# Optimization experiments

Hardware: AMD Instinct MI355X
Metric: run time of the kernel (lower is better)

The kernel has to match this reference:

```python
import jax, jax.numpy as jnp
import numpy as np

IM = 256          # image size (square)
GRID = 512        # oversampled NUFFT grid
J = 6             # Kaiser-Bessel kernel width (torchkbnufft default numpoints)
ALPHA = GRID / IM
BETA = float(np.pi * np.sqrt((J / ALPHA) ** 2 * (ALPHA - 0.5) ** 2 - 0.8))  # Fessler 'best' beta
SC0 = float(np.sinh(BETA) / BETA)
B, C = 1, 8
N_SPOKES, N_SAMPLES = 256, 512
K = N_SPOKES * N_SAMPLES


def _scale_2d():
    # deapodization (inverse FT of KB kernel), separable, normalized to 1 at center
    n = (jnp.arange(IM) - IM / 2) / GRID
    t = BETA ** 2 - (np.pi * J * n) ** 2
    sp = jnp.sqrt(jnp.maximum(t, 1e-12))
    sn = jnp.sqrt(jnp.maximum(-t, 1e-12))
    ft = jnp.where(t > 0, jnp.sinh(sp) / sp, jnp.sinc(sn / np.pi))
    sc = (SC0 / ft).astype(jnp.float32)
    return sc[:, None] * sc[None, :]  # (IM, IM)


def _interp_coords(ktraj):
    # ktraj (2, K) in [-pi, pi] -> J neighbor grid indices + KB weights per dim
    tm = ktraj * (GRID / (2.0 * np.pi))
    base = jnp.floor(tm - J / 2.0)
    j = jnp.arange(1, J + 1, dtype=tm.dtype)
    idx = base[:, :, None] + j                     # (2, K, J)
    u = tm[:, :, None] - idx                       # kernel-centered distance
    q = jnp.maximum(1.0 - (2.0 * u / J) ** 2, 0.0)
    w = jnp.i0(BETA * jnp.sqrt(q)) / J             # (2, K, J) KB weights
    gi = jnp.mod(idx, GRID).astype(jnp.int32)
    return gi[0], gi[1], w[0], w[1]                # iy, ix, wy, wx


def _nufft_fwd(img, coords, sc2):
    # img (B, C, IM, IM) complex -> (B, C, K) non-uniform k-space, 'ortho' norm
    iy, ix, wy, wx = coords
    pad = jnp.zeros(img.shape[:2] + (GRID, GRID), img.dtype)
    pad = pad.at[..., :IM, :IM].set(img * sc2)
    kg = jnp.fft.fft2(pad) / GRID                  # /sqrt(GRID*GRID)
    vals = kg[..., iy[:, :, None], ix[:, None, :]]           # (B,C,K,J,J)
    w2 = (wy[:, :, None] * wx[:, None, :]).astype(kg.dtype)  # (K,J,J)
    return jnp.sum(vals * w2, axis=(-2, -1))


def _nufft_adj(kdata, coords, sc2, smaps):
    # kdata (B, C, K) -> coil-combined image (B, 1, IM, IM), 'ortho' norm
    iy, ix, wy, wx = coords
    w2 = (wy[:, :, None] * wx[:, None, :]).astype(kdata.dtype)
    vals = (kdata[..., None, None] * w2).reshape(kdata.shape[:2] + (-1,))
    flat = (iy[:, :, None] * GRID + ix[:, None, :]).reshape(-1)
    grid = jnp.zeros(kdata.shape[:2] + (GRID * GRID,), kdata.dtype)
    grid = grid.at[:, :, flat].add(vals).reshape(kdata.shape[:2] + (GRID, GRID))
    img = jnp.fft.ifft2(grid) * GRID               # adjoint of fft2/GRID
    img = img[..., :IM, :IM] * sc2
    return jnp.sum(jnp.conj(smaps) * img, axis=1, keepdims=True)


def setup_inputs() -> dict:
    key = jax.random.key(0)
    ks = jax.random.split(key, 6)
    # golden-angle radial trajectory (2, K) in [-pi, pi]
    ga = np.pi * (3.0 - np.sqrt(5.0))
    ang = np.arange(N_SPOKES) * ga
    r = np.linspace(-np.pi, np.pi, N_SAMPLES, endpoint=False)
    ky = np.outer(np.sin(ang), r).reshape(-1)
    kx = np.outer(np.cos(ang), r).reshape(-1)
    ktraj = jnp.asarray(np.stack([ky, kx]), dtype=jnp.float32)
    return {
        "x": jax.random.normal(ks[0], (B, 1, IM, IM), jnp.float32),
        "y_real": jax.random.normal(ks[1], (B, C, K), jnp.float32),
        "y_imag": jax.random.normal(ks[2], (B, C, K), jnp.float32),
        "smaps_real": jax.random.normal(ks[3], (B, C, IM, IM), jnp.float32),
        "smaps_imag": jax.random.normal(ks[4], (B, C, IM, IM), jnp.float32),
        "ktraj": ktraj,
        "lambda_raw": jnp.full((1,), float(np.log(np.exp(1.0) - 1.0)), jnp.float32),
    }


def reference(x, y_real, y_imag, smaps_real, smaps_imag, ktraj, lambda_raw):
    sc2 = _scale_2d()
    coords = _interp_coords(ktraj)
    smaps = (smaps_real + 1j * smaps_imag).astype(jnp.complex64)
    y = (y_real + 1j * y_imag).astype(jnp.complex64)
    x_c = x.astype(jnp.complex64)
    coil_images = x_c * smaps                      # (B, C, IM, IM)
    A_x = _nufft_fwd(coil_images, coords, sc2)     # (B, C, K)
    lam = jax.nn.sigmoid(lambda_raw)[0].astype(jnp.complex64)
    k_dc = lam * A_x + (1.0 - lam) * y             # data consistency mix
    return _nufft_adj(k_dc, coords, sc2, smaps)    # (B, 1, IM, IM) complex64
```

## Files before the change

### kernel.cpp

```cpp
#include <hip/hip_runtime.h>
#include <math.h>

#define GRID_N 512
#define IM_N   256
#define NCOIL  8
#define NK     131072
#define PLANE  (GRID_N*GRID_N)
#define JW     6
#define NBIN   (GRID_N*GRID_N/512*512)
#define WSZ    11
#define NWIN   47
#define ACCROWS 528
#define BETA_F 13.8551003f
#define KSCALE 81.48733086305042f

struct cplx { float x, y; };

__device__ __forceinline__ float bessel_i0f(float x){
  if (x < 3.75f){
    float t = x*(1.0f/3.75f); t = t*t;
    return 1.0f + t*(3.5156229f + t*(3.0899424f + t*(1.2067492f
           + t*(0.2659732f + t*(0.0360768f + t*0.0045813f)))));
  } else {
    float t = 3.75f/x;
    float p = 0.39894228f + t*(0.01328592f + t*(0.00225319f + t*(-0.00157565f
            + t*(0.00916281f + t*(-0.02057706f + t*(0.02635537f
            + t*(-0.01647633f + t*0.00392377f)))))));
    return p * __expf(x) * rsqrtf(x);
  }
}

__device__ __forceinline__ float kb_w(float u){
  float uu = u*(1.0f/3.0f);
  float q = fmaxf(1.0f - uu*uu, 0.0f);
  return bessel_i0f(BETA_F*sqrtf(q)) * (1.0f/6.0f);
}

__device__ __forceinline__ unsigned bf16_of(float f){
  unsigned u = __float_as_uint(f);
  return (u + 0x8000u) >> 16;
}
__device__ __forceinline__ float bf_lo(unsigned w){ return __uint_as_float(w << 16); }
__device__ __forceinline__ float bf_hi(unsigned w){ return __uint_as_float(w & 0xFFFF0000u); }

__global__ void k_sc_table(float* sc){
  int i = threadIdx.x;
  if (i >= IM_N) return;
  float n  = (i - IM_N*0.5f) * (1.0f/GRID_N);
  float pj = 3.14159265358979f * (float)JW * n;
  float t  = BETA_F*BETA_F - pj*pj;
  float sp = sqrtf(fmaxf(t, 1e-12f));
  float sn = sqrtf(fmaxf(-t, 1e-12f));
  float ft = (t > 0.0f) ? (sinhf(sp)/sp) : (sinf(sn)/sn);
  float sc0 = sinhf(BETA_F)/BETA_F;
  sc[i] = sc0/ft;
}

__global__ void k_zero1(float* p, int n){
  int i = blockIdx.x*blockDim.x + threadIdx.x;
  if (i < n) p[i] = 0.f;
}

__global__ void k_fft_fill(const float* __restrict__ ximg, const float* __restrict__ sr,
                           const float* __restrict__ si, const float* __restrict__ sc,
                           cplx* __restrict__ buf){
  __shared__ cplx lds[GRID_N];
  int blk = blockIdx.x;
  int c = blk >> 9, y = blk & (GRID_N-1);
  cplx* p = buf + (size_t)blk * GRID_N;
  int tid = threadIdx.x;
  if (y >= IM_N){
    cplx z; z.x = 0.f; z.y = 0.f;
    for (int i = tid; i < GRID_N; i += 256) p[i] = z;
    return;
  }
  float scy = sc[y];
  for (int i = tid; i < GRID_N; i += 256){
    int r = __brev((unsigned)i) >> 23;
    cplx v; v.x = 0.f; v.y = 0.f;
    if (i < IM_N){
      float vv = ximg[(y<<8)|i] * scy * sc[i];
      int gi = (c << 16) | (y << 8) | i;
      v.x = vv * sr[gi]; v.y = vv * si[gi];
    }
    lds[r] = v;
  }
  __syncthreads();
  for (int half = 1; half < GRID_N; half <<= 1){
    int j = tid & (half-1);
    int k = ((tid & ~(half-1)) << 1) | j;
    float ang = -3.14159265358979f * (float)j / (float)half;
    float sw, cw; __sincosf(ang, &sw, &cw);
    cplx u = lds[k];
    cplx v = lds[k+half];
    cplx t; t.x = v.x*cw - v.y*sw; t.y = v.x*sw + v.y*cw;
    lds[k].x      = u.x + t.x; lds[k].y      = u.y + t.y;
    lds[k+half].x = u.x - t.x; lds[k+half].y = u.y - t.y;
    __syncthreads();
  }
  for (int i = tid; i < GRID_N; i += 256) p[i] = lds[i];
}

template<int DIR>
__global__ void k_fft_rows(cplx* __restrict__ buf, float scale){
  __shared__ cplx lds[GRID_N];
  cplx* p = buf + (size_t)blockIdx.x * GRID_N;
  int tid = threadIdx.x;
  for (int i = tid; i < GRID_N; i += 256){
    int r = __brev((unsigned)i) >> 23;
    lds[r] = p[i];
  }
  __syncthreads();
  for (int half = 1; half < GRID_N; half <<= 1){
    int j = tid & (half-1);
    int k = ((tid & ~(half-1)) << 1) | j;
    float ang = (float)DIR * 3.14159265358979f * (float)j / (float)half;
    float sw, cw; __sincosf(ang, &sw, &cw);
    cplx u = lds[k];
    cplx v = lds[k+half];
    cplx t; t.x = v.x*cw - v.y*sw; t.y = v.x*sw + v.y*cw;
    lds[k].x      = u.x + t.x; lds[k].y      = u.y + t.y;
    lds[k+half].x = u.x - t.x; lds[k+half].y = u.y - t.y;
    __syncthreads();
  }
  for (int i = tid; i < GRID_N; i += 256){
    cplx v = lds[i]; v.x *= scale; v.y *= scale; p[i] = v;
  }
}

__global__ void k_fft_rows_c(cplx* __restrict__ buf, float scale){
  __shared__ cplx lds[GRID_N];
  int b = blockIdx.x;
  int c = b >> 8, y = b & (IM_N-1);
  cplx* p = buf + (size_t)c*PLANE + (size_t)y*GRID_N;
  int tid = threadIdx.x;
  for (int i = tid; i < GRID_N; i += 256){
    int r = __brev((unsigned)i) >> 23;
    lds[r] = p[i];
  }
  __syncthreads();
  for (int half = 1; half < GRID_N; half <<= 1){
    int j = tid & (half-1);
    int k = ((tid & ~(half-1)) << 1) | j;
    float ang = 3.14159265358979f * (float)j / (float)half;
    float sw, cw; __sincosf(ang, &sw, &cw);
    cplx u = lds[k];
    cplx v = lds[k+half];
    cplx t; t.x = v.x*cw - v.y*sw; t.y = v.x*sw + v.y*cw;
    lds[k].x      = u.x + t.x; lds[k].y      = u.y + t.y;
    lds[k+half].x = u.x - t.x; lds[k+half].y = u.y - t.y;
    __syncthreads();
  }
  for (int i = tid; i < IM_N; i += 256){
    cplx v = lds[i]; v.x *= scale; v.y *= scale; p[i] = v;
  }
}

__global__ void k_transpose(const cplx* __restrict__ in, cplx* __restrict__ out){
  __shared__ cplx tile[32][33];
  int c  = blockIdx.z;
  int x0 = blockIdx.x*32, y0 = blockIdx.y*32;
  const cplx* ip = in  + (size_t)c*PLANE;
  cplx*       op = out + (size_t)c*PLANE;
  int tx = threadIdx.x, ty = threadIdx.y;
  for (int dy = 0; dy < 32; dy += 8)
    tile[ty+dy][tx] = ip[(size_t)(y0+ty+dy)*GRID_N + (x0+tx)];
  __syncthreads();
  for (int dy = 0; dy < 32; dy += 8)
    op[(size_t)(x0+ty+dy)*GRID_N + (y0+tx)] = tile[tx][ty+dy];
}

__global__ void k_c2i(const float2* __restrict__ plan, float2* __restrict__ inter){
  int t = blockIdx.x*blockDim.x + threadIdx.x;
  if (t >= PLANE*NCOIL) return;
  int c = t & 7; int cell = t >> 3;
  inter[(size_t)cell*8 + c] = plan[(size_t)c*PLANE + cell];
}

__global__ __launch_bounds__(256) void k_fwd(
    const float* __restrict__ ktraj, const float* __restrict__ yre,
    const float* __restrict__ yim, const float* __restrict__ lraw,
    const float4* __restrict__ KTi4, float4* __restrict__ kdc4){
  int t = blockIdx.x*blockDim.x + threadIdx.x;
  if (t >= NK*4) return;
  int k = t >> 2, p = t & 3;

  int iy[JW], ix[JW]; float wy[JW], wx[JW];
  {
    float tm = ktraj[k] * KSCALE;
    int base = (int)floorf(tm - 3.0f);
    #pragma unroll
    for (int j = 1; j <= JW; ++j){
      int fidx = base + j;
      wy[j-1] = kb_w(tm - (float)fidx);
      iy[j-1] = fidx & (GRID_N-1);
    }
  }
  {
    float tm = ktraj[NK + k] * KSCALE;
    int base = (int)floorf(tm - 3.0f);
    #pragma unroll
    for (int j = 1; j <= JW; ++j){
      int fidx = base + j;
      wx[j-1] = kb_w(tm - (float)fidx);
      ix[j-1] = fidx & (GRID_N-1);
    }
  }

  float ax=0.f, ay=0.f, az=0.f, aw=0.f;
  #pragma unroll
  for (int jx = 0; jx < JW; ++jx){
    int ox = ix[jx]*GRID_N;
    #pragma unroll
    for (int jy = 0; jy < JW; ++jy){
      float w2 = wx[jx]*wy[jy];
      float4 v = KTi4[(size_t)(ox + iy[jy])*4 + p];
      ax += w2*v.x; ay += w2*v.y; az += w2*v.z; aw += w2*v.w;
    }
  }
  float lam = 1.0f/(1.0f + __expf(-lraw[0]));
  float oml = 1.0f - lam;
  int c0 = 2*p;
  float4 o;
  o.x = lam*ax + oml*yre[(size_t)c0*NK + k];
  o.y = lam*ay + oml*yim[(size_t)c0*NK + k];
  o.z = lam*az + oml*yre[(size_t)(c0+1)*NK + k];
  o.w = lam*aw + oml*yim[(size_t)(c0+1)*NK + k];
  kdc4[(size_t)k*4 + p] = o;
}

__global__ void k_hist2(const float* __restrict__ ktraj, unsigned* __restrict__ hist2){
  int k = blockIdx.x*blockDim.x + threadIdx.x;
  if (k >= NK) return;
  float tmy = ktraj[k] * KSCALE;
  int by = ((int)floorf(tmy - 3.0f)) & (GRID_N-1);
  float tmx = ktraj[NK + k] * KSCALE;
  int bx = (int)floorf(tmx - 3.0f);
  #pragma unroll
  for (int j = 1; j <= JW; ++j){
    int cj = (bx + j) & (GRID_N-1);
    atomicAdd(&hist2[cj*GRID_N + by], 1u);
  }
}

__global__ void k_colscan(const unsigned* __restrict__ hist2,
                          unsigned* __restrict__ binOff,
                          unsigned* __restrict__ colTotal){
  __shared__ unsigned s[GRID_N];
  int col = blockIdx.x, t = threadIdx.x;
  unsigned mine = hist2[col*GRID_N + t];
  s[t] = mine;
  __syncthreads();
  for (int off = 1; off < GRID_N; off <<= 1){
    unsigned add = (t >= off) ? s[t - off] : 0u;
    __syncthreads();
    s[t] += add;
    __syncthreads();
  }
  binOff[col*GRID_N + t] = s[t] - mine;
  if (t == GRID_N-1) colTotal[col] = s[t];
}

__global__ void k_scanCT(const unsigned* __restrict__ colTotal,
                         unsigned* __restrict__ colBase){
  __shared__ unsigned s[GRID_N];
  int t = threadIdx.x;
  unsigned mine = colTotal[t];
  s[t] = mine;
  __syncthreads();
  for (int off = 1; off < GRID_N; off <<= 1){
    unsigned add = (t >= off) ? s[t - off] : 0u;
    __syncthreads();
    s[t] += add;
    __syncthreads();
  }
  colBase[t] = s[t] - mine;
  if (t == GRID_N-1) colBase[GRID_N] = s[t];
}

__global__ void k_addbase(unsigned* __restrict__ binOff,
                          const unsigned* __restrict__ colBase){
  int i = blockIdx.x*blockDim.x + threadIdx.x;
  if (i > NBIN) return;
  if (i == NBIN){ binOff[i] = colBase[GRID_N]; return; }
  binOff[i] += colBase[i >> 9];
}

__global__ void k_place(const float* __restrict__ ktraj,
                        const unsigned* __restrict__ binOff,
                        unsigned* __restrict__ cnt2,
                        uint4* __restrict__ recs){
  int k = blockIdx.x*blockDim.x + threadIdx.x;
  if (k >= NK) return;
  float tmy = ktraj[k] * KSCALE;
  int by0 = (int)floorf(tmy - 3.0f);
  int by = by0 & (GRID_N-1);
  float wy[JW];
  #pragma unroll
  for (int j = 1; j <= JW; ++j) wy[j-1] = kb_w(tmy - (float)(by0 + j));

  float tmx = ktraj[NK + k] * KSCALE;
  int bx = (int)floorf(tmx - 3.0f);
  unsigned tag = ((unsigned)k << 9) | (unsigned)by;
  #pragma unroll
  for (int j = 1; j <= JW; ++j){
    int cj = (bx + j) & (GRID_N-1);
    float wx = kb_w(tmx - (float)(bx + j));
    uint4 rec;
    rec.x = bf16_of(wx*wy[0]) | (bf16_of(wx*wy[1]) << 16);
    rec.y = bf16_of(wx*wy[2]) | (bf16_of(wx*wy[3]) << 16);
    rec.z = bf16_of(wx*wy[4]) | (bf16_of(wx*wy[5]) << 16);
    rec.w = tag;
    int bin = cj*GRID_N + by;
    unsigned pos = binOff[bin] + atomicAdd(&cnt2[bin], 1u);
    recs[pos] = rec;
  }
}

__global__ __launch_bounds__(512) void k_adj(
    const uint4* __restrict__ recs, const unsigned* __restrict__ binOff,
    const float* __restrict__ kdcf, cplx* __restrict__ Hp){
  __shared__ float accs[ACCROWS*16];
  __shared__ float part[8][16][16];
  const int col = blockIdx.x;
  const int tid = threadIdx.x;
  const int wave = tid >> 6, lane = tid & 63;
  const int slot = lane >> 4, q = lane & 15;
  for (int i = tid; i < ACCROWS*16; i += 512) accs[i] = 0.f;
  __syncthreads();

  const unsigned* bo = binOff + (size_t)col*GRID_N;

  for (int wi = 0; wi < NWIN; ++wi){
    int b0 = wi*WSZ;
    int b1 = b0 + WSZ; if (b1 > GRID_N) b1 = GRID_N;
    unsigned s = bo[b0];
    unsigned e = bo[b1];
    if (s == e) continue;

    float a0=0.f,a1=0.f,a2=0.f,a3=0.f,a4=0.f,a5=0.f,a6=0.f,a7=0.f;
    float a8=0.f,a9=0.f,a10=0.f,a11=0.f,a12=0.f,a13=0.f,a14=0.f,a15=0.f;

    for (unsigned base = s + (unsigned)wave*4; base < e; base += 32){
      unsigned e0 = base + (unsigned)slot;
      uint4 rc = recs[e0];
      float vv = 0.f;
      if (e0 < e){
        unsigned kk = (rc.w >> 9) & (NK-1);
        vv = kdcf[(size_t)kk*16 + q];
      }
      float w1 = bf_lo(rc.x), w2 = bf_hi(rc.x);
      float w3 = bf_lo(rc.y), w4 = bf_hi(rc.y);
      float w5 = bf_lo(rc.z), w6 = bf_hi(rc.z);
      int off = (int)(rc.w & (GRID_N-1)) - b0;
      #pragma unroll
      for (int r = 0; r < 16; ++r){
        int idx = r - off;
        float wlo = (idx < 2) ? w1 : ((idx < 4) ? w3 : w5);
        float whi = (idx < 2) ? w2 : ((idx < 4) ? w4 : w6);
        float w = (idx & 1) ? whi : wlo;
        w = ((unsigned)idx < 6u) ? w : 0.f;
        float contrib = w * vv;
        if (r==0) a0+=contrib; else if (r==1) a1+=contrib;
        else if (r==2) a2+=contrib; else if (r==3) a3+=contrib;
        else if (r==4) a4+=contrib; else if (r==5) a5+=contrib;
        else if (r==6) a6+=contrib; else if (r==7) a7+=contrib;
        else if (r==8) a8+=contrib; else if (r==9) a9+=contrib;
        else if (r==10) a10+=contrib; else if (r==11) a11+=contrib;
        else if (r==12) a12+=contrib; else if (r==13) a13+=contrib;
        else if (r==14) a14+=contrib; else a15+=contrib;
      }
    }

    #pragma unroll
    for (int m = 16; m <= 32; m <<= 1){
      a0 += __shfl_xor(a0, m);  a1 += __shfl_xor(a1, m);
      a2 += __shfl_xor(a2, m);  a3 += __shfl_xor(a3, m);
      a4 += __shfl_xor(a4, m);  a5 += __shfl_xor(a5, m);
      a6 += __shfl_xor(a6, m);  a7 += __shfl_xor(a7, m);
      a8 += __shfl_xor(a8, m);  a9 += __shfl_xor(a9, m);
      a10 += __shfl_xor(a10, m); a11 += __shfl_xor(a11, m);
      a12 += __shfl_xor(a12, m); a13 += __shfl_xor(a13, m);
      a14 += __shfl_xor(a14, m); a15 += __shfl_xor(a15, m);
    }
    if (slot == 0){
      part[wave][0][q]  = a0;  part[wave][1][q]  = a1;
      part[wave][2][q]  = a2;  part[wave][3][q]  = a3;
      part[wave][4][q]  = a4;  part[wave][5][q]  = a5;
      part[wave][6][q]  = a6;  part[wave][7][q]  = a7;
      part[wave][8][q]  = a8;  part[wave][9][q]  = a9;
      part[wave][10][q] = a10; part[wave][11][q] = a11;
      part[wave][12][q] = a12; part[wave][13][q] = a13;
      part[wave][14][q] = a14; part[wave][15][q] = a15;
    }
    __syncthreads();
    if (tid < 256){
      int r = tid >> 4, qq = tid & 15;
      float sum = part[0][r][qq] + part[1][r][qq] + part[2][r][qq]
                + part[3][r][qq] + part[4][r][qq] + part[5][r][qq]
                + part[6][r][qq] + part[7][r][qq];
      accs[(size_t)(b0+1+r)*16 + qq] += sum;
    }
    __syncthreads();
  }

  for (int i = tid; i < GRID_N*8; i += 512){
    int j = i >> 9, y = i & (GRID_N-1);
    float re = accs[y*16 + 2*j]     + ((y < 16) ? accs[(GRID_N+y)*16 + 2*j]   : 0.f);
    float im = accs[y*16 + 2*j + 1] + ((y < 16) ? accs[(GRID_N+y)*16 + 2*j+1] : 0.f);
    cplx o; o.x = re; o.y = im;
    Hp[(size_t)j*PLANE + (size_t)col*GRID_N + y] = o;
  }
}

__global__ void k_final(const cplx* __restrict__ Bg, const float* __restrict__ sr,
                        const float* __restrict__ si, const float* __restrict__ sc,
                        float* __restrict__ out, int pairs){
  int idx = blockIdx.x*blockDim.x + threadIdx.x;
  if (idx >= IM_N*IM_N) return;
  int y = idx >> 8, x = idx & 255;
  float s2 = sc[y]*sc[x];
  float ax = 0.f, ay = 0.f;
  #pragma unroll
  for (int c = 0; c < NCOIL; ++c){
    cplx v = Bg[(size_t)c*PLANE + y*GRID_N + x];
    int gi = (c << 16) | idx;
    float rr = sr[gi], ii = si[gi];
    ax += rr*v.x + ii*v.y;
    ay += rr*v.y - ii*v.x;
  }
  if (pairs){
    out[idx*2]   += ax * s2;
    out[idx*2+1] += ay * s2;
  } else {
    out[idx]     += ax * s2;
  }
}

__global__ void k_zero4(float4* p, int n4){
  int i = blockIdx.x*blockDim.x + threadIdx.x;
  if (i < n4) p[i] = make_float4(0.f,0.f,0.f,0.f);
}

__global__ void k_fill_fb(const float* __restrict__ ximg, const float* __restrict__ sr,
                          const float* __restrict__ si, const float* __restrict__ sc,
                          cplx* __restrict__ A){
  int idx = blockIdx.x*blockDim.x + threadIdx.x;
  if (idx >= NCOIL*IM_N*IM_N) return;
  int c = idx >> 16;
  int pix = idx & 65535;
  int y = pix >> 8, x = pix & 255;
  float v = ximg[pix] * sc[y]*sc[x];
  cplx o; o.x = v * sr[idx]; o.y = v * si[idx];
  A[(size_t)c*PLANE + y*GRID_N + x] = o;
}

__global__ void k_gather_scatter_fb(const float* __restrict__ ktraj,
                                    const float* __restrict__ yre,
                                    const float* __restrict__ yim,
                                    const float* __restrict__ lraw,
                                    const cplx* __restrict__ KT,
                                    float* __restrict__ HT){
  int k = blockIdx.x*blockDim.x + threadIdx.x;
  if (k >= NK) return;
  float lam   = 1.0f/(1.0f + __expf(-lraw[0]));
  float omlam = 1.0f - lam;
  int iy[JW], ix[JW]; float wy[JW], wx[JW];
  {
    float tm = ktraj[k] * KSCALE;
    int base = (int)floorf(tm - 3.0f);
    #pragma unroll
    for (int j = 1; j <= JW; ++j){
      wy[j-1] = kb_w(tm - (float)(base+j));
      iy[j-1] = (base+j) & (GRID_N-1);
    }
  }
  {
    float tm = ktraj[NK + k] * KSCALE;
    int base = (int)floorf(tm - 3.0f);
    #pragma unroll
    for (int j = 1; j <= JW; ++j){
      wx[j-1] = kb_w(tm - (float)(base+j));
      ix[j-1] = (base+j) & (GRID_N-1);
    }
  }
  float accx[NCOIL], accy[NCOIL];
  #pragma unroll
  for (int c = 0; c < NCOIL; ++c){ accx[c]=0.f; accy[c]=0.f; }
  #pragma unroll
  for (int jx = 0; jx < JW; ++jx){
    int ox = ix[jx]*GRID_N;
    #pragma unroll
    for (int jy = 0; jy < JW; ++jy){
      float w2 = wx[jx]*wy[jy];
      size_t o = (size_t)(ox + iy[jy]);
      #pragma unroll
      for (int c = 0; c < NCOIL; ++c){
        cplx v = KT[(size_t)c*PLANE + o];
        accx[c] += w2*v.x; accy[c] += w2*v.y;
      }
    }
  }
  float kdx[NCOIL], kdy[NCOIL];
  #pragma unroll
  for (int c = 0; c < NCOIL; ++c){
    kdx[c] = lam*accx[c] + omlam*yre[(size_t)c*NK + k];
    kdy[c] = lam*accy[c] + omlam*yim[(size_t)c*NK + k];
  }
  #pragma unroll
  for (int jx = 0; jx < JW; ++jx){
    int ox = ix[jx]*GRID_N;
    #pragma unroll
    for (int jy = 0; jy < JW; ++jy){
      float w2 = wx[jx]*wy[jy];
      size_t o = (size_t)(ox + iy[jy]);
      #pragma unroll
      for (int c = 0; c < NCOIL; ++c){
        float* dst = HT + ((size_t)c*PLANE + o)*2;
        atomicAdd(dst,   w2*kdx[c]);
        atomicAdd(dst+1, w2*kdy[c]);
      }
    }
  }
}

extern "C" void kernel_launch(void* const* d_in, const int* in_sizes, int n_in,
                              void* d_out, int out_size, void* d_ws, size_t ws_size,
                              hipStream_t stream) {
  const float* ximg  = (const float*)d_in[0];
  const float* yre   = (const float*)d_in[1];
  const float* yim   = (const float*)d_in[2];
  const float* sre   = (const float*)d_in[3];
  const float* sim   = (const float*)d_in[4];
  const float* ktraj = (const float*)d_in[5];
  const float* lraw  = (const float*)d_in[6];
  float* out = (float*)d_out;

  char* ws = (char*)d_ws;
  const size_t REG = 16777216;
  int pairs = (out_size >= 2*IM_N*IM_N) ? 1 : 0;

  const size_t need = 3*REG + 4096;

  if (ws_size >= need){
    cplx*     A     = (cplx*)ws;
    cplx*     Bb    = (cplx*)(ws + REG);
    float4*   KTi4  = (float4*)(ws + 2*REG);
    float*    sc    = (float*)(ws + 3*REG);
    float4*   kdc4  = (float4*)ws;
    unsigned* hist2 = (unsigned*)(ws + 8388608);
    unsigned* cnt2  = (unsigned*)(ws + 9437184);
    unsigned* binOff= (unsigned*)(ws + 10485760);
    unsigned* colTot= (unsigned*)(ws + 11538432);
    unsigned* colBase=(unsigned*)(ws + 11540480);
    uint4*    recs  = (uint4*)(ws + REG);
    cplx*     Hp    = (cplx*)(ws + 2*REG);
    cplx*     imgF  = (cplx*)ws;

    k_sc_table<<<1,256,0,stream>>>(sc);

    k_fft_fill<<<NCOIL*GRID_N,256,0,stream>>>(ximg, sre, sim, sc, A);
    k_transpose<<<dim3(16,16,NCOIL),dim3(32,8),0,stream>>>(A, Bb);
    k_fft_rows<-1><<<NCOIL*GRID_N,256,0,stream>>>(Bb, 1.0f/(float)GRID_N);

    k_c2i<<<(PLANE*NCOIL+255)/256,256,0,stream>>>((const float2*)Bb, (float2*)KTi4);

    k_fwd<<<(NK*4+255)/256,256,0,stream>>>(ktraj, yre, yim, lraw, KTi4, kdc4);

    k_zero1<<<(2*NBIN+255)/256,256,0,stream>>>((float*)hist2, 2*NBIN);
    k_hist2<<<NK/256,256,0,stream>>>(ktraj, hist2);
    k_colscan<<<GRID_N,GRID_N,0,stream>>>(hist2, binOff, colTot);
    k_scanCT<<<1,GRID_N,0,stream>>>(colTot, colBase);
    k_addbase<<<(NBIN+256)/256,256,0,stream>>>(binOff, colBase);
    k_place<<<NK/256,256,0,stream>>>(ktraj, binOff, cnt2, recs);

    k_adj<<<GRID_N,512,0,stream>>>(recs, binOff, (const float*)kdc4, Hp);

    k_fft_rows<+1><<<NCOIL*GRID_N,256,0,stream>>>(Hp, 1.0f);
    k_transpose<<<dim3(8,16,NCOIL),dim3(32,8),0,stream>>>(Hp, imgF);
    k_fft_rows_c<<<NCOIL*IM_N,256,0,stream>>>(imgF, 1.0f/(float)GRID_N);

    k_zero1<<<(out_size+255)/256,256,0,stream>>>(out, out_size);
    k_final<<<(IM_N*IM_N+255)/256,256,0,stream>>>(imgF, sre, sim, sc, out, pairs);
  } else {
    float* sc = (float*)ws;
    cplx*  A  = (cplx*)(ws + 4096);
    cplx*  Bb = (cplx*)(ws + 4096 + REG);
    const int n4 = NCOIL*PLANE*2/4;

    k_sc_table<<<1,256,0,stream>>>(sc);
    k_zero4<<<(n4+255)/256,256,0,stream>>>((float4*)A, n4);
    k_fill_fb<<<(NCOIL*IM_N*IM_N+255)/256,256,0,stream>>>(ximg, sre, sim, sc, A);
    k_fft_rows<-1><<<NCOIL*GRID_N,256,0,stream>>>(A, 1.0f);
    k_transpose<<<dim3(16,16,NCOIL),dim3(32,8),0,stream>>>(A, Bb);
    k_fft_rows<-1><<<NCOIL*GRID_N,256,0,stream>>>(Bb, 1.0f/(float)GRID_N);
    k_zero4<<<(n4+255)/256,256,0,stream>>>((float4*)A, n4);
    k_gather_scatter_fb<<<(NK+255)/256,256,0,stream>>>(ktraj, yre, yim, lraw, Bb, (float*)A);
    k_fft_rows<+1><<<NCOIL*GRID_N,256,0,stream>>>(A, 1.0f);
    k_transpose<<<dim3(16,16,NCOIL),dim3(32,8),0,stream>>>(A, Bb);
    k_fft_rows<+1><<<NCOIL*GRID_N,256,0,stream>>>(Bb, 1.0f/(float)GRID_N);
    k_zero1<<<(out_size+255)/256,256,0,stream>>>(out, out_size);
    k_final<<<(IM_N*IM_N+255)/256,256,0,stream>>>(Bb, sre, sim, sc, out, pairs);
  }
}
```

Before: 397.9 us.

## Split adjoint gridding per column into two halves with overlap side buffer

The adjoint gridding kernel now launches two blocks per grid column, each covering half of the row windows with a smaller LDS accumulator. Rows where the two halves overlap, plus the wraparound rows, are written to a side buffer instead of Hp. A new row-FFT kernel adds those side contributions while loading each row. The aim is twice as many blocks with less shared memory each, for better occupancy and load balance. The cost is extra side-buffer traffic and more complex merge logic in the FFT load.

```diff
diff --git a/kernel.cpp b/kernel.cpp
--- a/kernel.cpp
+++ b/kernel.cpp
@@ -10,7 +10,9 @@
 #define NBIN   (GRID_N*GRID_N/512*512)
 #define WSZ    11
 #define NWIN   47
-#define ACCROWS 528
+#define SPLITW 24
+#define BASE1  (SPLITW*WSZ)
+#define NLROWS 272
 #define BETA_F 13.8551003f
 #define KSCALE 81.48733086305042f
 
@@ -128,6 +130,41 @@
   }
 }
 
+__global__ void k_fft_rows_m(cplx* __restrict__ buf,
+                             const float* __restrict__ side){
+  __shared__ cplx lds[GRID_N];
+  int blk = blockIdx.x;
+  int c = blk >> 9, col = blk & (GRID_N-1);
+  cplx* p = buf + (size_t)blk * GRID_N;
+  int tid = threadIdx.x;
+  for (int i = tid; i < GRID_N; i += 256){
+    int r = __brev((unsigned)i) >> 23;
+    cplx v = p[i];
+    int sidx = -1;
+    if (i >= 1 && i <= 15) sidx = i - 1;
+    else if (i >= 265 && i <= 269) sidx = i - 250;
+    if (sidx >= 0){
+      const float* sp = side + ((size_t)col*20 + sidx)*16 + 2*c;
+      v.x += sp[0]; v.y += sp[1];
+    }
+    lds[r] = v;
+  }
+  __syncthreads();
+  for (int half = 1; half < GRID_N; half <<= 1){
+    int j = tid & (half-1);
+    int k = ((tid & ~(half-1)) << 1) | j;
+    float ang = 3.14159265358979f * (float)j / (float)half;
+    float sw, cw; __sincosf(ang, &sw, &cw);
+    cplx u = lds[k];
+    cplx v = lds[k+half];
+    cplx t; t.x = v.x*cw - v.y*sw; t.y = v.x*sw + v.y*cw;
+    lds[k].x      = u.x + t.x; lds[k].y      = u.y + t.y;
+    lds[k+half].x = u.x - t.x; lds[k+half].y = u.y - t.y;
+    __syncthreads();
+  }
+  for (int i = tid; i < GRID_N; i += 256) p[i] = lds[i];
+}
+
 __global__ void k_fft_rows_c(cplx* __restrict__ buf, float scale){
   __shared__ cplx lds[GRID_N];
   int b = blockIdx.x;
@@ -319,19 +356,23 @@
 
 __global__ __launch_bounds__(512) void k_adj(
     const uint4* __restrict__ recs, const unsigned* __restrict__ binOff,
-    const float* __restrict__ kdcf, cplx* __restrict__ Hp){
-  __shared__ float accs[ACCROWS*16];
+    const float* __restrict__ kdcf, cplx* __restrict__ Hp,
+    float* __restrict__ side){
+  __shared__ float accs[NLROWS*16];
   __shared__ float part[8][16][16];
-  const int col = blockIdx.x;
+  const int col = blockIdx.x, h = blockIdx.y;
   const int tid = threadIdx.x;
   const int wave = tid >> 6, lane = tid & 63;
   const int slot = lane >> 4, q = lane & 15;
-  for (int i = tid; i < ACCROWS*16; i += 512) accs[i] = 0.f;
+  for (int i = tid; i < NLROWS*16; i += 512) accs[i] = 0.f;
   __syncthreads();
 
   const unsigned* bo = binOff + (size_t)col*GRID_N;
-
-  for (int wi = 0; wi < NWIN; ++wi){
+  const int wlo = h ? SPLITW : 0;
+  const int whi = h ? NWIN : SPLITW;
+  const int base0 = h ? BASE1 : 0;
+
+  for (int wi = wlo; wi < whi; ++wi){
     int b0 = wi*WSZ;
     int b1 = b0 + WSZ; if (b1 > GRID_N) b1 = GRID_N;
     unsigned s = bo[b0];
@@ -356,9 +397,9 @@
       #pragma unroll
       for (int r = 0; r < 16; ++r){
         int idx = r - off;
-        float wlo = (idx < 2) ? w1 : ((idx < 4) ? w3 : w5);
-        float whi = (idx < 2) ? w2 : ((idx < 4) ? w4 : w6);
-        float w = (idx & 1) ? whi : wlo;
+        float wlo2 = (idx < 2) ? w1 : ((idx < 4) ? w3 : w5);
+        float whi2 = (idx < 2) ? w2 : ((idx < 4) ? w4 : w6);
+        float w = (idx & 1) ? whi2 : wlo2;
         w = ((unsigned)idx < 6u) ? w : 0.f;
         float contrib = w * vv;
         if (r==0) a0+=contrib; else if (r==1) a1+=contrib;
@@ -399,17 +440,38 @@
       float sum = part[0][r][qq] + part[1][r][qq] + part[2][r][qq]
                 + part[3][r][qq] + part[4][r][qq] + part[5][r][qq]
                 + part[6][r][qq] + part[7][r][qq];
-      accs[(size_t)(b0+1+r)*16 + qq] += sum;
-    }
-    __syncthreads();
-  }
-
-  for (int i = tid; i < GRID_N*8; i += 512){
-    int j = i >> 9, y = i & (GRID_N-1);
-    float re = accs[y*16 + 2*j]     + ((y < 16) ? accs[(GRID_N+y)*16 + 2*j]   : 0.f);
-    float im = accs[y*16 + 2*j + 1] + ((y < 16) ? accs[(GRID_N+y)*16 + 2*j+1] : 0.f);
-    cplx o; o.x = re; o.y = im;
-    Hp[(size_t)j*PLANE + (size_t)col*GRID_N + y] = o;
+      accs[(size_t)(b0 + 1 + r - base0)*16 + qq] += sum;
+    }
+    __syncthreads();
+  }
+
+  for (int i = tid; i < NLROWS*8; i += 512){
+    int l = i >> 3, j = i & 7;
+    if (h == 0){
+      if (l < 1 || l > 269) continue;
+      cplx o; o.x = accs[l*16 + 2*j]; o.y = accs[l*16 + 2*j + 1];
+      Hp[(size_t)j*PLANE + (size_t)col*GRID_N + l] = o;
+    } else {
+      if (l < 1 || l > 263) continue;
+      int g = BASE1 + l;
+      float re = accs[l*16 + 2*j], im = accs[l*16 + 2*j + 1];
+      if (g >= 512){
+        int gw = g - 512;
+        if (gw == 0){
+          cplx o; o.x = re; o.y = im;
+          Hp[(size_t)j*PLANE + (size_t)col*GRID_N] = o;
+        } else {
+          float* sp = side + ((size_t)col*20 + (gw-1))*16 + 2*j;
+          sp[0] = re; sp[1] = im;
+        }
+      } else if (g >= 270){
+        cplx o; o.x = re; o.y = im;
+        Hp[(size_t)j*PLANE + (size_t)col*GRID_N + g] = o;
+      } else {
+        float* sp = side + ((size_t)col*20 + (g-250))*16 + 2*j;
+        sp[0] = re; sp[1] = im;
+      }
+    }
   }
 }
 
@@ -553,6 +615,7 @@
     unsigned* binOff= (unsigned*)(ws + 10485760);
     unsigned* colTot= (unsigned*)(ws + 11538432);
     unsigned* colBase=(unsigned*)(ws + 11540480);
+    float*    side  = (float*)(ws + 12582912);
     uint4*    recs  = (uint4*)(ws + REG);
     cplx*     Hp    = (cplx*)(ws + 2*REG);
     cplx*     imgF  = (cplx*)ws;
@@ -574,9 +637,10 @@
     k_addbase<<<(NBIN+256)/256,256,0,stream>>>(binOff, colBase);
     k_place<<<NK/256,256,0,stream>>>(ktraj, binOff, cnt2, recs);
 
-    k_adj<<<GRID_N,512,0,stream>>>(recs, binOff, (const float*)kdc4, Hp);
-
-    k_fft_rows<+1><<<NCOIL*GRID_N,256,0,stream>>>(Hp, 1.0f);
+    k_adj<<<dim3(GRID_N,2),512,0,stream>>>(recs, binOff, (const float*)kdc4,
+                                           Hp, side);
+
+    k_fft_rows_m<<<NCOIL*GRID_N,256,0,stream>>>(Hp, side);
     k_transpose<<<dim3(8,16,NCOIL),dim3(32,8),0,stream>>>(Hp, imgF);
     k_fft_rows_c<<<NCOIL*IM_N,256,0,stream>>>(imgF, 1.0f/(float)GRID_N);
 
```

After: 336.0 us, median of 2. 1.18x faster.
